# Kernel optimization log

Measured on AMD Instinct MI355X. Metric: run time of the kernel, lower is better.

The kernel has to match this reference:

```python
import jax, jax.numpy as jnp
import numpy as np

D = 1024; H = 16; DKV = 64; DFF = 4096
NB = 32; MAXD = 128
B = 4; LD = 1024; LE = 1024
NEG = -1e9
EPS = 1e-6


def setup_inputs():
    key = jax.random.key(0)
    ks = jax.random.split(key, 13)
    s = 0.02
    def W(k, shape):
        return jax.random.normal(k, shape, jnp.float32) * s
    return {
        "encoder_hidden_states": jax.random.normal(ks[0], (B, LE, D), jnp.float32),
        "hidden_states": jax.random.normal(ks[1], (B, LD, D), jnp.float32),
        "ln1_w": jnp.ones((D,), jnp.float32),
        "sa_q": W(ks[2], (D, H * DKV)),
        "sa_k": W(ks[3], (D, H * DKV)),
        "sa_v": W(ks[4], (D, H * DKV)),
        "sa_o": W(ks[5], (H * DKV, D)),
        "rel_bias": W(ks[6], (NB, H)),
        "ln2_w": jnp.ones((D,), jnp.float32),
        "ca_q": W(ks[7], (D, H * DKV)),
        "ca_k": W(ks[8], (D, H * DKV)),
        "ca_v": W(ks[9], (D, H * DKV)),
        "ca_o": W(ks[10], (H * DKV, D)),
        "ln3_w": jnp.ones((D,), jnp.float32),
        "wi": W(ks[11], (D, DFF)),
        "wo": W(ks[12], (DFF, D)),
        "final_ln_w": jnp.ones((D,), jnp.float32),
        "encoder_attention_mask": jnp.ones((B, LE), jnp.int32),
        "attention_mask": jnp.ones((B, LD), jnp.int32),
    }


def _rms(x, w):
    # T5 LayerNorm: RMS norm, no mean subtraction, no bias
    var = jnp.mean(x * x, axis=-1, keepdims=True)
    return x * jax.lax.rsqrt(var + EPS) * w


def _rel_bucket(rp):
    # T5 relative position bucketing, non-bidirectional (decoder causal)
    n = -jnp.minimum(rp, 0)
    max_exact = NB // 2
    is_small = n < max_exact
    nf = jnp.maximum(n, 1).astype(jnp.float32)
    val_large = max_exact + (
        jnp.log(nf / max_exact) / np.log(MAXD / max_exact) * (NB - max_exact)
    ).astype(jnp.int32)
    val_large = jnp.minimum(val_large, NB - 1)
    return jnp.where(is_small, n, val_large)


def _attn(xq, xkv, Wq, Wk, Wv, Wo, bias):
    b, lq, _ = xq.shape
    lk = xkv.shape[1]
    q = (xq @ Wq).reshape(b, lq, H, DKV)
    k = (xkv @ Wk).reshape(b, lk, H, DKV)
    v = (xkv @ Wv).reshape(b, lk, H, DKV)
    # T5: no 1/sqrt(d) scaling; additive position bias + mask before softmax
    scores = jnp.einsum('bqhd,bkhd->bhqk', q, k) + bias
    p = jax.nn.softmax(scores, axis=-1)
    o = jnp.einsum('bhqk,bkhd->bqhd', p, v).reshape(b, lq, H * DKV)
    return o @ Wo


def reference(encoder_hidden_states, hidden_states, ln1_w, sa_q, sa_k, sa_v, sa_o,
              rel_bias, ln2_w, ca_q, ca_k, ca_v, ca_o, ln3_w, wi, wo, final_ln_w,
              encoder_attention_mask, attention_mask):
    b, ld, _ = hidden_states.shape
    q_pos = jnp.arange(ld)[:, None]
    k_pos = jnp.arange(ld)[None, :]
    pos_bias = rel_bias[_rel_bucket(k_pos - q_pos)].transpose(2, 0, 1)[None]  # [1,H,LD,LD]
    # decoder extended mask: causal AND padding
    self_ok = (k_pos <= q_pos)[None, None] & (attention_mask[:, None, None, :] > 0)
    self_bias = pos_bias + jnp.where(self_ok, 0.0, NEG)
    # cross-attention: encoder padding mask; enc-dec position bias is zeros
    cross_bias = jnp.where(encoder_attention_mask[:, None, None, :] > 0, 0.0, NEG)

    h = hidden_states
    x = _rms(h, ln1_w)
    h = h + _attn(x, x, sa_q, sa_k, sa_v, sa_o, self_bias)
    x = _rms(h, ln2_w)
    h = h + _attn(x, encoder_hidden_states, ca_q, ca_k, ca_v, ca_o, cross_bias)
    x = _rms(h, ln3_w)
    h = h + jax.nn.relu(x @ wi) @ wo
    return _rms(h, final_ln_w)
```

## Files before the change

### kernel.cpp

```cpp
#include <hip/hip_runtime.h>


#define BB   4
#define LDEC 1024
#define LENC 1024
#define DIM  1024
#define NH   16
#define DK   64
#define DFFN 4096
#define NEGF (-1e9f)

typedef unsigned short u16;
typedef __attribute__((ext_vector_type(8))) unsigned short u16x8;
typedef __attribute__((ext_vector_type(8))) short s16x8;
typedef __attribute__((ext_vector_type(4))) float f32x4;

__device__ __forceinline__ float bf2f(u16 u) {
    union { unsigned int i; float f; } c; c.i = ((unsigned int)u) << 16; return c.f;
}
__device__ __forceinline__ u16 f2bf(float f) {
    union { float f; unsigned int i; } c; c.f = f;
    unsigned int x = c.i;
    return (u16)((x + 0x7fffu + ((x >> 16) & 1u)) >> 16);
}
__device__ __forceinline__ bool probe_f32(const void* probe) {
    return ((const u16*)probe)[0] != 0x3F80;
}
__device__ __forceinline__ float ldx(const void* p, long i, bool f32) {
    return f32 ? ((const float*)p)[i] : bf2f(((const u16*)p)[i]);
}
__device__ __forceinline__ float4 ldx4(const void* p, long i, bool f32) {
    if (f32) return ((const float4*)p)[i >> 2];
    ushort4 u = ((const ushort4*)p)[i >> 2];
    return make_float4(bf2f(u.x), bf2f(u.y), bf2f(u.z), bf2f(u.w));
}
__device__ __forceinline__ void stx(void* p, long i, float v, bool f32) {
    if (f32) ((float*)p)[i] = v;
    else     ((u16*)p)[i] = f2bf(v);
}

__device__ __forceinline__ void gload16(const void* g, void* l) {
    __builtin_amdgcn_global_load_lds(
        (const __attribute__((address_space(1))) void*)g,
        (__attribute__((address_space(3))) void*)l, 16, 0, 0);
}

__global__ __launch_bounds__(256) void copy_k(const void* __restrict__ src,
                                              void* __restrict__ dst,
                                              const void* __restrict__ probe, int n) {
    bool pf = probe_f32(probe);
    long bytes = (long)n * (pf ? 4 : 2);
    long off = ((long)blockIdx.x * 256 + threadIdx.x) * 16;
    if (off < bytes)
        *(int4*)((char*)dst + off) = *(const int4*)((const char*)src + off);
}

__global__ __launch_bounds__(256) void cvt_k(const void* __restrict__ src,
                                             u16* __restrict__ dst,
                                             const void* __restrict__ probe, int n4) {
    bool pf = probe_f32(probe);
    int i = blockIdx.x * 256 + threadIdx.x;
    if (i >= n4) return;
    if (pf) {
        float4 f = ((const float4*)src)[i];
        ushort4 o;
        o.x = f2bf(f.x); o.y = f2bf(f.y); o.z = f2bf(f.z); o.w = f2bf(f.w);
        ((ushort4*)dst)[i] = o;
    } else {
        ((ushort4*)dst)[i] = ((const ushort4*)src)[i];
    }
}

struct TPack {
    const void* s[10]; void* d[10];
    int K[10], N[10], t0[11];
};
__global__ __launch_bounds__(256) void transp_k(TPack p, const void* __restrict__ probe) {
    bool pf = probe_f32(probe);
    __shared__ u16 tl[32][33];
    int bid = blockIdx.x;
    int w = 0;
    while (bid >= p.t0[w + 1]) ++w;
    int lt = bid - p.t0[w];
    const int K = p.K[w], N = p.N[w];
    const int ntx = N >> 5;
    const int bn = (lt % ntx) * 32, bk = (lt / ntx) * 32;
    const int c = threadIdx.x & 31, rr = threadIdx.x >> 5;
    const void* s = p.s[w];
    u16* d = (u16*)p.d[w];
#pragma unroll
    for (int i = 0; i < 4; ++i) {
        int r = rr + i * 8;
        long gi = (long)(bk + r) * N + bn + c;
        tl[c][r] = pf ? f2bf(((const float*)s)[gi]) : ((const u16*)s)[gi];
    }
    __syncthreads();
#pragma unroll
    for (int i = 0; i < 4; ++i) {
        int r = rr + i * 8;
        d[(long)(bn + r) * K + bk + c] = tl[r][c];
    }
}

template <int XM, int YM, int CP>
__global__ __launch_bounds__(256) void rms_k(const void* __restrict__ X,
                                             const void* __restrict__ w,
                                             void* __restrict__ Y,
                                             void* __restrict__ R,
                                             const void* __restrict__ probe,
                                             long xoff, long yoff) {
    bool pf = probe_f32(probe);
    bool xf = XM && pf, yf = YM && pf;
    const int row = blockIdx.x, t = threadIdx.x;
    const long idx = (long)row * DIM + t * 4;
    float4 xv = ldx4(X, xoff + idx, xf);
    float ss = xv.x * xv.x;
    ss = fmaf(xv.y, xv.y, ss);
    ss = fmaf(xv.z, xv.z, ss);
    ss = fmaf(xv.w, xv.w, ss);
#pragma unroll
    for (int off = 32; off; off >>= 1) ss += __shfl_xor(ss, off, 64);
    __shared__ float part[4];
    if ((t & 63) == 0) part[t >> 6] = ss;
    __syncthreads();
    float tot = part[0] + part[1] + part[2] + part[3];
    float scale = rsqrtf(tot * (1.f / (float)DIM) + 1e-6f);
    float4 wv = ldx4(w, t * 4, pf);
    if (CP) {
        stx(R, idx + 0, xv.x, pf);
        stx(R, idx + 1, xv.y, pf);
        stx(R, idx + 2, xv.z, pf);
        stx(R, idx + 3, xv.w, pf);
    }
    stx(Y, yoff + idx + 0, xv.x * scale * wv.x, yf);
    stx(Y, yoff + idx + 1, xv.y * scale * wv.y, yf);
    stx(Y, yoff + idx + 2, xv.z * scale * wv.z, yf);
    stx(Y, yoff + idx + 3, xv.w * scale * wv.w, yf);
}

struct Gemm2Arg {
    const u16* A; const u16* BT; void* C;
    long aoff; long boff; long coff; int ldb;
};

template <int EPI, int BM>
__global__ __launch_bounds__(512) void mgemm2_k(Gemm2Arg g0, Gemm2Arg g1, Gemm2Arg g2,
                                                const void* __restrict__ probe,
                                                int M, int N, int K) {
    const bool pf = probe_f32(probe);
    Gemm2Arg ga = (blockIdx.z == 0) ? g0 : (blockIdx.z == 1 ? g1 : g2);
    constexpr int AG = BM / 64;
    constexpr int AFR = BM / 32;

    __shared__ u16 Asm[2][BM * 64];
    __shared__ u16 Bsm[2][128 * 64];

    const int tid = threadIdx.x;
    const int nx = gridDim.x;
    const int nwg = nx * gridDim.y;
    const int L = blockIdx.x + nx * blockIdx.y;
    const int tile = (L & 7) * (nwg >> 3) + (L >> 3);
    const int m_base = (tile / nx) * BM, n_base = (tile % nx) * 128;

    const int w = tid >> 6, lane = tid & 63;
    const int wm = w >> 2, wn = w & 3;
    const int l15 = lane & 15, quad = lane >> 4;
    const int arow8 = lane >> 3;
    const int acg = (lane & 7) ^ arow8;

    const int iters = K >> 6;
    const u16* Ab = ga.A + ga.aoff;
    const u16* Bb = ga.BT + ga.boff;

#pragma unroll
    for (int g = 0; g < AG; ++g)
        gload16(Ab + (long)(m_base + w * (BM / 8) + g * 8 + arow8) * K + acg * 8,
                &Asm[0][(w * (BM / 8) + g * 8) * 64]);
#pragma unroll
    for (int g = 0; g < 2; ++g)
        gload16(Bb + (long)(n_base + w * 16 + g * 8 + arow8) * ga.ldb + acg * 8,
                &Bsm[0][(w * 16 + g * 8) * 64]);

    f32x4 acc[AFR][2] = {};
    int cur = 0;
    for (int it = 0; it < iters; ++it) {
        __syncthreads();
        if (it + 1 < iters) {
            const int k0 = (it + 1) << 6;
#pragma unroll
            for (int g = 0; g < AG; ++g)
                gload16(Ab + (long)(m_base + w * (BM / 8) + g * 8 + arow8) * K + k0 + acg * 8,
                        &Asm[cur ^ 1][(w * (BM / 8) + g * 8) * 64]);
#pragma unroll
            for (int g = 0; g < 2; ++g)
                gload16(Bb + (long)(n_base + w * 16 + g * 8 + arow8) * ga.ldb + k0 + acg * 8,
                        &Bsm[cur ^ 1][(w * 16 + g * 8) * 64]);
        }
#pragma unroll
        for (int s = 0; s < 2; ++s) {
            s16x8 afr[AFR], bfr[2];
#pragma unroll
            for (int i = 0; i < AFR; ++i) {
                int row = wm * (BM / 2) + i * 16 + l15;
                int chunk = ((s << 2) | quad) ^ (row & 7);
                afr[i] = *(const s16x8*)&Asm[cur][row * 64 + chunk * 8];
            }
#pragma unroll
            for (int j = 0; j < 2; ++j) {
                int nr = wn * 32 + j * 16 + l15;
                int chunk = ((s << 2) | quad) ^ (nr & 7);
                bfr[j] = *(const s16x8*)&Bsm[cur][nr * 64 + chunk * 8];
            }
#pragma unroll
            for (int i = 0; i < AFR; ++i)
#pragma unroll
                for (int j = 0; j < 2; ++j)
                    acc[i][j] = __builtin_amdgcn_mfma_f32_16x16x32_bf16(
                        afr[i], bfr[j], acc[i][j], 0, 0, 0);
        }
        cur ^= 1;
    }

#pragma unroll
    for (int i = 0; i < AFR; ++i) {
#pragma unroll
        for (int j = 0; j < 2; ++j) {
            int n = n_base + wn * 32 + j * 16 + l15;
#pragma unroll
            for (int r4 = 0; r4 < 4; ++r4) {
                int m = m_base + wm * (BM / 2) + i * 16 + quad * 4 + r4;
                float v = acc[i][j][r4];
                if (EPI == 1) v = fmaxf(v, 0.f);
                long cidx = ga.coff + (long)m * N + n;
                if (EPI == 2) {
                    v += ldx(ga.C, cidx, pf);
                    stx(ga.C, cidx, v, pf);
                } else {
                    ((u16*)ga.C)[cidx] = f2bf(v);
                }
            }
        }
    }
}

struct GemmArg {
    const void* A; const void* B; void* C;
    long aoff; long boff; long coff; int asrc; int bsrc; int ldb;
};

__device__ __forceinline__ void load_breg(const GemmArg& ga, bool bf, int k0,
                                          int bk2, int bnb, int n_base, u16* breg) {
    long base0 = (long)(k0 + bk2) * ga.ldb + ga.boff + n_base + bnb;
    long base1 = base0 + ga.ldb;
    if (bf) {
        const float4* Bf = (const float4*)ga.B;
#pragma unroll
        for (int r = 0; r < 2; ++r) {
            long b = (r ? base1 : base0) >> 2;
#pragma unroll
            for (int c = 0; c < 2; ++c) {
                float4 f = Bf[b + c];
                breg[r * 8 + c * 4 + 0] = f2bf(f.x);
                breg[r * 8 + c * 4 + 1] = f2bf(f.y);
                breg[r * 8 + c * 4 + 2] = f2bf(f.z);
                breg[r * 8 + c * 4 + 3] = f2bf(f.w);
            }
        }
    } else {
        u16x8 v0 = *(const u16x8*)((const u16*)ga.B + base0);
        u16x8 v1 = *(const u16x8*)((const u16*)ga.B + base1);
#pragma unroll
        for (int i = 0; i < 8; ++i) { breg[i] = v0[i]; breg[8 + i] = v1[i]; }
    }
}

template <int EPI>
__global__ __launch_bounds__(512) void mgemm_k(GemmArg g0, GemmArg g1, GemmArg g2,
                                               const void* __restrict__ probe,
                                               int M, int N, int K) {
    const bool pf = probe_f32(probe);
    GemmArg ga = (blockIdx.z == 0) ? g0 : (blockIdx.z == 1 ? g1 : g2);
    const bool af = (ga.asrc >= 1) && pf;
    const bool bf = (ga.bsrc >= 1) && pf;

    __shared__ u16 Asm[2][128 * 64];
    __shared__ u16 Bsm[128 * 64];

    const int tid = threadIdx.x;
    const int nx = gridDim.x;
    const int nwg = nx * gridDim.y;
    const int L = blockIdx.x + nx * blockIdx.y;
    const int tile = (L & 7) * (nwg >> 3) + (L >> 3);
    const int m_base = (tile / nx) * 128, n_base = (tile % nx) * 128;

    const int w = tid >> 6, lane = tid & 63;
    const int wm = w >> 2, wn = w & 3;
    const int l15 = lane & 15, quad = lane >> 4;

    const int bk2 = (tid & 31) * 2;
    const int bnb = (tid >> 5) * 8;
    const int arow8 = lane >> 3;
    const int acg = (lane & 7) ^ arow8;

    const int iters = K >> 6;
    u16 breg[16];
    load_breg(ga, bf, 0, bk2, bnb, n_base, breg);
    if (!af) {
#pragma unroll
        for (int g = 0; g < 2; ++g) {
            const u16* Ag = (const u16*)ga.A + ga.aoff +
                            (long)(m_base + w * 16 + g * 8 + arow8) * K + acg * 8;
            gload16(Ag, &Asm[0][(w * 16 + g * 8) * 64]);
        }
    }

    f32x4 acc[4][2] = {};

    for (int it = 0; it < iters; ++it) {
        const int cur = it & 1;
        __syncthreads();
        if (af) {
            const int row = tid >> 2;
            const float4* Af = (const float4*)ga.A;
            long gb = ga.aoff + (long)(m_base + row) * K + (it << 6);
#pragma unroll
            for (int c = 0; c < 2; ++c) {
                int cg = (tid & 3) * 2 + c;
                float4 fa = Af[(gb + cg * 8) >> 2];
                float4 fb = Af[((gb + cg * 8) >> 2) + 1];
                u16x8 o;
                o[0] = f2bf(fa.x); o[1] = f2bf(fa.y); o[2] = f2bf(fa.z); o[3] = f2bf(fa.w);
                o[4] = f2bf(fb.x); o[5] = f2bf(fb.y); o[6] = f2bf(fb.z); o[7] = f2bf(fb.w);
                *(u16x8*)&Asm[cur][row * 64 + ((cg ^ (row & 7)) << 3)] = o;
            }
        }
#pragma unroll
        for (int i = 0; i < 8; ++i) {
            int n = bnb + i;
            unsigned int pr = (unsigned int)breg[i] | ((unsigned int)breg[8 + i] << 16);
            *(unsigned int*)&Bsm[n * 64 + (((bk2 >> 3) ^ (n & 7)) << 3) + (bk2 & 7)] = pr;
        }
        __syncthreads();
        if (it + 1 < iters) {
            load_breg(ga, bf, (it + 1) << 6, bk2, bnb, n_base, breg);
            if (!af) {
#pragma unroll
                for (int g = 0; g < 2; ++g) {
                    const u16* Ag = (const u16*)ga.A + ga.aoff +
                                    (long)(m_base + w * 16 + g * 8 + arow8) * K +
                                    ((it + 1) << 6) + acg * 8;
                    gload16(Ag, &Asm[cur ^ 1][(w * 16 + g * 8) * 64]);
                }
            }
        }
#pragma unroll
        for (int s = 0; s < 2; ++s) {
            s16x8 afr[4], bfr[2];
#pragma unroll
            for (int i = 0; i < 4; ++i) {
                int row = wm * 64 + i * 16 + l15;
                int chunk = ((s << 2) | quad) ^ (row & 7);
                afr[i] = *(const s16x8*)&Asm[cur][row * 64 + chunk * 8];
            }
#pragma unroll
            for (int j = 0; j < 2; ++j) {
                int nr = wn * 32 + j * 16 + l15;
                int chunk = ((s << 2) | quad) ^ (nr & 7);
                bfr[j] = *(const s16x8*)&Bsm[nr * 64 + chunk * 8];
            }
#pragma unroll
            for (int i = 0; i < 4; ++i)
#pragma unroll
                for (int j = 0; j < 2; ++j)
                    acc[i][j] = __builtin_amdgcn_mfma_f32_16x16x32_bf16(
                        afr[i], bfr[j], acc[i][j], 0, 0, 0);
        }
    }

#pragma unroll
    for (int i = 0; i < 4; ++i) {
#pragma unroll
        for (int j = 0; j < 2; ++j) {
            int n = n_base + wn * 32 + j * 16 + l15;
#pragma unroll
            for (int r4 = 0; r4 < 4; ++r4) {
                int m = m_base + wm * 64 + i * 16 + quad * 4 + r4;
                float v = acc[i][j][r4];
                if (EPI == 1) v = fmaxf(v, 0.f);
                long cidx = ga.coff + (long)m * N + n;
                if (EPI == 2) {
                    v += ldx(ga.C, cidx, pf);
                    stx(ga.C, cidx, v, pf);
                } else {
                    ((u16*)ga.C)[cidx] = f2bf(v);
                }
            }
        }
    }
}

template <int SELF>
__global__ __launch_bounds__(256) void fattn_k(const u16* __restrict__ Q,
                                               const u16* __restrict__ K,
                                               const u16* __restrict__ V,
                                               const void* __restrict__ relb,
                                               const int* __restrict__ mask,
                                               u16* __restrict__ O,
                                               const void* __restrict__ probe,
                                               int LK, int b0, int bufrows) {
    const bool pf = probe_f32(probe);
    __shared__ u16 Ks[64][72];
    __shared__ u16 Vt[64][72];
    __shared__ u16 Ps[64][72];
    __shared__ float bias_lut[SELF ? 1024 : 1];

    const int t = threadIdx.x;
    const int lane = t & 63, w = t >> 6;
    const int l15 = lane & 15, quad = lane >> 4;

    int x, h, z;
    if (gridDim.z == 4) {
        int lid = blockIdx.x + (int)gridDim.x * (blockIdx.y + (int)gridDim.y * blockIdx.z);
        int q = lid >> 8, r = lid & 255, a = r & 3;
        x = (q == 0) ? a : (q == 1) ? 15 - a : (q == 2) ? 4 + a : 11 - a;
        h = (r >> 2) & 15;
        z = r >> 6;
    } else {
        x = blockIdx.x; h = blockIdx.y; z = blockIdx.z;
    }
    const int q0 = x * 64;
    const int batch = b0 + z;
    const long bv = (long)z * bufrows * DIM;
    const int* mrow = mask + batch * LK;

    if (SELF) {
        for (int i = t; i < 1024; i += 256) {
            int bucket;
            if (i < 16) bucket = i;
            else {
                int vv = 16 + (int)(logf((float)i * 0.0625f) * 7.69436394f);
                bucket = vv < 31 ? vv : 31;
            }
            bias_lut[i] = ldx(relb, bucket * NH + h, pf);
        }
    }

    s16x8 qf[2];
    {
        const u16* qp = Q + bv + (long)(q0 + w * 16 + l15) * DIM + h * DK + quad * 8;
        qf[0] = *(const s16x8*)qp;
        qf[1] = *(const s16x8*)(qp + 32);
    }

    float l_reg[4] = {0.f, 0.f, 0.f, 0.f};
    f32x4 Oa[4] = {};

    const int ntiles = SELF ? (q0 >> 6) + 1 : (LK >> 6);
    const int kr = t >> 2, kseg = t & 3;
    const int kr2 = (t & 31) * 2, dnb = (t >> 5) * 8;

    u16x8 kp0, kp1, vp0, vp1;
    {
        long gb = bv + (long)kr * DIM + h * DK + kseg * 16;
        kp0 = *(const u16x8*)(K + gb);
        kp1 = *(const u16x8*)(K + gb + 8);
        long gv = bv + (long)kr2 * DIM + h * DK + dnb;
        vp0 = *(const u16x8*)(V + gv);
        vp1 = *(const u16x8*)(V + gv + DIM);
    }

    for (int kt = 0; kt < ntiles; ++kt) {
        __syncthreads();
        *(u16x8*)&Ks[kr][kseg * 16] = kp0;
        *(u16x8*)&Ks[kr][kseg * 16 + 8] = kp1;
#pragma unroll
        for (int i = 0; i < 8; ++i) {
            unsigned int pr = (unsigned int)vp0[i] | ((unsigned int)vp1[i] << 16);
            *(unsigned int*)&Vt[dnb + i][kr2] = pr;
        }
        __syncthreads();
        if (kt + 1 < ntiles) {
            long gb = bv + (long)((kt + 1) * 64 + kr) * DIM + h * DK + kseg * 16;
            kp0 = *(const u16x8*)(K + gb);
            kp1 = *(const u16x8*)(K + gb + 8);
            long gv = bv + (long)((kt + 1) * 64 + kr2) * DIM + h * DK + dnb;
            vp0 = *(const u16x8*)(V + gv);
            vp1 = *(const u16x8*)(V + gv + DIM);
        }

        f32x4 sc[4] = {};
#pragma unroll
        for (int j = 0; j < 4; ++j)
#pragma unroll
            for (int s = 0; s < 2; ++s) {
                s16x8 bf = *(const s16x8*)&Ks[j * 16 + l15][s * 32 + quad * 8];
                sc[j] = __builtin_amdgcn_mfma_f32_16x16x32_bf16(qf[s], bf, sc[j], 0, 0, 0);
            }

#pragma unroll
        for (int j = 0; j < 4; ++j) {
            int key = kt * 64 + j * 16 + l15;
            float ma = (mrow[key] > 0) ? 0.f : NEGF;
#pragma unroll
            for (int r = 0; r < 4; ++r) {
                float sv = sc[j][r];
                if (SELF) {
                    int q = q0 + w * 16 + quad * 4 + r;
                    int d = q - key;
                    sv += bias_lut[d < 0 ? 0 : d] + ((key <= q) ? ma : NEGF);
                } else {
                    sv += ma;
                }
                float p = __expf(sv);
                Ps[w * 16 + quad * 4 + r][j * 16 + l15] = f2bf(p);
                l_reg[r] += p;
            }
        }
        asm volatile("" ::: "memory");

#pragma unroll
        for (int s = 0; s < 2; ++s) {
            s16x8 pa = *(const s16x8*)&Ps[w * 16 + l15][s * 32 + quad * 8];
#pragma unroll
            for (int j = 0; j < 4; ++j) {
                s16x8 vb = *(const s16x8*)&Vt[j * 16 + l15][s * 32 + quad * 8];
                Oa[j] = __builtin_amdgcn_mfma_f32_16x16x32_bf16(pa, vb, Oa[j], 0, 0, 0);
            }
        }
    }

#pragma unroll
    for (int r = 0; r < 4; ++r) {
        float v = l_reg[r];
        v += __shfl_xor(v, 1, 64);
        v += __shfl_xor(v, 2, 64);
        v += __shfl_xor(v, 4, 64);
        v += __shfl_xor(v, 8, 64);
        l_reg[r] = 1.f / v;
    }
#pragma unroll
    for (int j = 0; j < 4; ++j)
#pragma unroll
        for (int r = 0; r < 4; ++r) {
            int row = w * 16 + quad * 4 + r;
            O[bv + (long)(q0 + row) * DIM + h * DK + j * 16 + l15] =
                f2bf(Oa[j][r] * l_reg[r]);
        }
}

extern "C" void kernel_launch(void* const* d_in, const int* in_sizes, int n_in,
                              void* d_out, int out_size, void* d_ws, size_t ws_size,
                              hipStream_t stream) {
    const void* enc  = d_in[0];
    const void* hs   = d_in[1];
    const void* ln1  = d_in[2];
    const void* sa_q = d_in[3];
    const void* sa_k = d_in[4];
    const void* sa_v = d_in[5];
    const void* sa_o = d_in[6];
    const void* relb = d_in[7];
    const void* ln2  = d_in[8];
    const void* ca_q = d_in[9];
    const void* ca_k = d_in[10];
    const void* ca_v = d_in[11];
    const void* ca_o = d_in[12];
    const void* ln3  = d_in[13];
    const void* wi   = d_in[14];
    const void* wo   = d_in[15];
    const void* fln  = d_in[16];
    const int* enc_mask = (const int*)d_in[17];
    const int* dec_mask = (const int*)d_in[18];
    void* out = d_out;
    const void* probe = ln1;

    char* ws = (char*)d_ws;
    const int M = BB * LDEC;
    dim3 blk(256), blkG(512);
    GemmArg dz = {nullptr, nullptr, nullptr, 0, 0, 0, 0, 0, 0};
    Gemm2Arg dz2 = {nullptr, nullptr, nullptr, 0, 0, 0, 0};

    if (ws_size >= (72ull << 20)) {
        u16* X0 = (u16*)(ws);
        u16* X1 = (u16*)(ws + (8u  << 20));
        u16* X2 = (u16*)(ws + (16u << 20));
        u16* X3 = (u16*)(ws + (24u << 20));
        u16* FF = X1;
        u16* encB = (u16*)(ws + (32u << 20));
        u16* wT[10];
        wT[0] = (u16*)(ws + (40u << 20));
        wT[1] = (u16*)(ws + (42u << 20));
        wT[2] = (u16*)(ws + (44u << 20));
        wT[3] = (u16*)(ws + (46u << 20));
        wT[4] = (u16*)(ws + (48u << 20));
        wT[5] = (u16*)(ws + (50u << 20));
        wT[6] = (u16*)(ws + (52u << 20));
        wT[7] = (u16*)(ws + (54u << 20));
        wT[8] = (u16*)(ws + (56u << 20));
        wT[9] = (u16*)(ws + (64u << 20));

        cvt_k<<<4096, blk, 0, stream>>>(enc, encB, probe, 1048576);
        {
            TPack p;
            const void* s[10] = {sa_q, sa_k, sa_v, sa_o, ca_q, ca_k, ca_v, ca_o, wi, wo};
            const int kk[10] = {DIM, DIM, DIM, DIM, DIM, DIM, DIM, DIM, DIM, DFFN};
            const int nn[10] = {DIM, DIM, DIM, DIM, DIM, DIM, DIM, DIM, DFFN, DIM};
            int acc = 0;
            for (int i = 0; i < 10; ++i) {
                p.s[i] = s[i]; p.d[i] = wT[i]; p.K[i] = kk[i]; p.N[i] = nn[i];
                p.t0[i] = acc; acc += (kk[i] >> 5) * (nn[i] >> 5);
            }
            p.t0[10] = acc;
            transp_k<<<acc, blk, 0, stream>>>(p, probe);
        }

        dim3 gQKV(8, 64, 3);
        dim3 gOP(8, 64, 1);
        dim3 gWI(16, 64, 2);
        dim3 gAttn(LDEC / 64, NH, BB);

        rms_k<1, 0, 1><<<M, blk, 0, stream>>>(hs, ln1, X0, out, probe, 0, 0);
        {
            Gemm2Arg zq = {X0, wT[0], X1, 0, 0, 0, DIM};
            Gemm2Arg zk = {X0, wT[1], X2, 0, 0, 0, DIM};
            Gemm2Arg zv = {X0, wT[2], X3, 0, 0, 0, DIM};
            mgemm2_k<0, 64><<<gQKV, blkG, 0, stream>>>(zq, zk, zv, probe, M, DIM, DIM);
        }
        fattn_k<1><<<gAttn, blk, 0, stream>>>(X1, X2, X3, relb, dec_mask, X0,
                                              probe, LDEC, 0, LDEC);
        {
            Gemm2Arg zo = {X0, wT[3], out, 0, 0, 0, DIM};
            mgemm2_k<2, 64><<<gOP, blkG, 0, stream>>>(zo, dz2, dz2, probe, M, DIM, DIM);
        }

        rms_k<1, 0, 0><<<M, blk, 0, stream>>>(out, ln2, X0, nullptr, probe, 0, 0);
        {
            Gemm2Arg zq = {X0, wT[4], X1, 0, 0, 0, DIM};
            Gemm2Arg zk = {encB, wT[5], X2, 0, 0, 0, DIM};
            Gemm2Arg zv = {encB, wT[6], X3, 0, 0, 0, DIM};
            mgemm2_k<0, 64><<<gQKV, blkG, 0, stream>>>(zq, zk, zv, probe, M, DIM, DIM);
        }
        fattn_k<0><<<gAttn, blk, 0, stream>>>(X1, X2, X3, relb, enc_mask, X0,
                                              probe, LENC, 0, LENC);
        {
            Gemm2Arg zo = {X0, wT[7], out, 0, 0, 0, DIM};
            mgemm2_k<2, 64><<<gOP, blkG, 0, stream>>>(zo, dz2, dz2, probe, M, DIM, DIM);
        }

        rms_k<1, 0, 0><<<M, blk, 0, stream>>>(out, ln3, X0, nullptr, probe, 0, 0);
        {
            Gemm2Arg z0 = {X0, wT[8], FF, 0, 0, 0, DIM};
            Gemm2Arg z1 = {X0, wT[8], FF, 0, (long)2048 * DIM, 2048, DIM};
            mgemm2_k<1, 64><<<gWI, blkG, 0, stream>>>(z0, z1, dz2, probe, M, DFFN, DIM);
        }
        {
            Gemm2Arg zo = {FF, wT[9], out, 0, 0, 0, DFFN};
            mgemm2_k<2, 64><<<gOP, blkG, 0, stream>>>(zo, dz2, dz2, probe, M, DIM, DFFN);
        }
    } else if (ws_size >= (32ull << 20)) {
        u16* X0 = (u16*)(ws);
        u16* X1 = (u16*)(ws + (8u << 20));
        u16* X2 = (u16*)(ws + (16u << 20));
        u16* X3 = (u16*)(ws + (24u << 20));
        u16* FF = X2;
        const bool have_encb = ws_size >= (40ull << 20);
        u16* encB = (u16*)(ws + (32u << 20));

        dim3 gQKV(8, 32, 3);
        dim3 gOP(8, 32, 1);
        dim3 gWI(16, 32, 1);
        dim3 gAttn(LDEC / 64, NH, BB);

        copy_k<<<(M * DIM / 4) / 256, blk, 0, stream>>>(hs, out, probe, M * DIM);
        if (have_encb)
            cvt_k<<<4096, blk, 0, stream>>>(enc, encB, probe, M * DIM / 4);

        rms_k<1, 0, 0><<<M, blk, 0, stream>>>(out, ln1, X0, nullptr, probe, 0, 0);
        {
            GemmArg zq = {X0, sa_q, X1, 0, 0, 0, 0, 1, DIM};
            GemmArg zk = {X0, sa_k, X2, 0, 0, 0, 0, 1, DIM};
            GemmArg zv = {X0, sa_v, X3, 0, 0, 0, 0, 1, DIM};
            mgemm_k<0><<<gQKV, blkG, 0, stream>>>(zq, zk, zv, probe, M, DIM, DIM);
        }
        fattn_k<1><<<gAttn, blk, 0, stream>>>(X1, X2, X3, relb, dec_mask, X0,
                                              probe, LDEC, 0, LDEC);
        {
            GemmArg zo = {X0, sa_o, out, 0, 0, 0, 0, 1, DIM};
            mgemm_k<2><<<gOP, blkG, 0, stream>>>(zo, dz, dz, probe, M, DIM, DIM);
        }

        rms_k<1, 0, 0><<<M, blk, 0, stream>>>(out, ln2, X0, nullptr, probe, 0, 0);
        {
            const void* encA = have_encb ? (const void*)encB : enc;
            int asrc = have_encb ? 0 : 1;
            GemmArg zq = {X0, ca_q, X1, 0, 0, 0, 0, 1, DIM};
            GemmArg zk = {encA, ca_k, X2, 0, 0, 0, asrc, 1, DIM};
            GemmArg zv = {encA, ca_v, X3, 0, 0, 0, asrc, 1, DIM};
            mgemm_k<0><<<gQKV, blkG, 0, stream>>>(zq, zk, zv, probe, M, DIM, DIM);
        }
        fattn_k<0><<<gAttn, blk, 0, stream>>>(X1, X2, X3, relb, enc_mask, X0,
                                              probe, LENC, 0, LENC);
        {
            GemmArg zo = {X0, ca_o, out, 0, 0, 0, 0, 1, DIM};
            mgemm_k<2><<<gOP, blkG, 0, stream>>>(zo, dz, dz, probe, M, DIM, DIM);
        }

        rms_k<1, 0, 0><<<M, blk, 0, stream>>>(out, ln3, X0, nullptr, probe, 0, 0);
        for (int d = 0; d < 2; ++d) {
            GemmArg zi = {X0, wi, FF, 0, (long)d * 2048, 0, 0, 1, DFFN};
            mgemm_k<1><<<gWI, blkG, 0, stream>>>(zi, dz, dz, probe, M, 2048, DIM);
            GemmArg zo = {FF, wo, out, 0, (long)d * 2048 * DIM, 0, 0, 1, DIM};
            mgemm_k<2><<<gOP, blkG, 0, stream>>>(zo, dz, dz, probe, M, DIM, 2048);
        }
    } else {
        u16* X0 = (u16*)(ws);
        u16* X1 = (u16*)(ws + (2u << 20));
        u16* X2 = (u16*)(ws + (4u << 20));
        u16* X3 = (u16*)(ws + (6u << 20));
        u16* XN = (u16*)(ws);
        u16* FF = (u16*)(ws + (4u << 20));
        dim3 gQKV(8, 8, 3);
        dim3 gOP(8, 8, 1);
        dim3 gFFN(8, 16, 1);
        dim3 gAttn(LDEC / 64, NH, 1);

        copy_k<<<(M * DIM / 4) / 256, blk, 0, stream>>>(hs, out, probe, M * DIM);

        for (int b = 0; b < BB; ++b) {
            const long ob = (long)b * LDEC * DIM;
            const long eb = (long)b * LENC * DIM;

            rms_k<1, 0, 0><<<LDEC, blk, 0, stream>>>(out, ln1, X0, nullptr, probe, ob, 0);
            {
                GemmArg zq = {X0, sa_q, X1, 0, 0, 0, 0, 1, DIM};
                GemmArg zk = {X0, sa_k, X2, 0, 0, 0, 0, 1, DIM};
                GemmArg zv = {X0, sa_v, X3, 0, 0, 0, 0, 1, DIM};
                mgemm_k<0><<<gQKV, blkG, 0, stream>>>(zq, zk, zv, probe, LDEC, DIM, DIM);
            }
            fattn_k<1><<<gAttn, blk, 0, stream>>>(X1, X2, X3, relb, dec_mask, X0,
                                                  probe, LDEC, b, 0);
            {
                GemmArg zo = {X0, sa_o, out, 0, 0, ob, 0, 1, DIM};
                mgemm_k<2><<<gOP, blkG, 0, stream>>>(zo, dz, dz, probe, LDEC, DIM, DIM);
            }

            rms_k<1, 0, 0><<<LDEC, blk, 0, stream>>>(out, ln2, X0, nullptr, probe, ob, 0);
            {
                GemmArg zq = {X0, ca_q, X1, 0, 0, 0, 0, 1, DIM};
                GemmArg zk = {enc, ca_k, X2, eb, 0, 0, 1, 1, DIM};
                GemmArg zv = {enc, ca_v, X3, eb, 0, 0, 1, 1, DIM};
                mgemm_k<0><<<gQKV, blkG, 0, stream>>>(zq, zk, zv, probe, LENC, DIM, DIM);
            }
            fattn_k<0><<<gAttn, blk, 0, stream>>>(X1, X2, X3, relb, enc_mask, X0,
                                                  probe, LENC, b, 0);
            {
                GemmArg zo = {X0, ca_o, out, 0, 0, ob, 0, 1, DIM};
                mgemm_k<2><<<gOP, blkG, 0, stream>>>(zo, dz, dz, probe, LDEC, DIM, DIM);
            }
        }

        for (int mc = 0; mc < 2; ++mc) {
            const long r0 = (long)mc * 2048;
            rms_k<1, 0, 0><<<2048, blk, 0, stream>>>(out, ln3, XN, nullptr, probe, r0 * DIM, 0);
            for (int d = 0; d < 4; ++d) {
                GemmArg zi = {XN, wi, FF, 0, (long)d * 1024, 0, 0, 1, DFFN};
                mgemm_k<1><<<gFFN, blkG, 0, stream>>>(zi, dz, dz, probe, 2048, 1024, DIM);
                GemmArg zo = {FF, wo, out, 0, (long)d * 1024 * DIM, r0 * DIM, 0, 1, DIM};
                mgemm_k<2><<<gFFN, blkG, 0, stream>>>(zo, dz, dz, probe, 2048, DIM, 1024);
            }
        }
    }

    rms_k<1, 1, 0><<<M, blk, 0, stream>>>(out, fln, out, nullptr, probe, 0, 0);
}
```

Baseline: 508.7 us.

## Triple-buffer GEMM shared memory with explicit vmcnt waits and raw barrier

```diff
diff --git a/kernel.cpp b/kernel.cpp
--- a/kernel.cpp
+++ b/kernel.cpp
@@ -151,9 +151,10 @@
     Gemm2Arg ga = (blockIdx.z == 0) ? g0 : (blockIdx.z == 1 ? g1 : g2);
     constexpr int AG = BM / 64;
     constexpr int AFR = BM / 32;
-
-    __shared__ u16 Asm[2][BM * 64];
-    __shared__ u16 Bsm[2][128 * 64];
+    static_assert(BM == 64, "vmcnt literal assumes 3 loads/tile");
+
+    __shared__ u16 Asm[3][BM * 64];
+    __shared__ u16 Bsm[3][128 * 64];
 
     const int tid = threadIdx.x;
     const int nx = gridDim.x;
@@ -172,30 +173,33 @@
     const u16* Ab = ga.A + ga.aoff;
     const u16* Bb = ga.BT + ga.boff;
 
-#pragma unroll
-    for (int g = 0; g < AG; ++g)
-        gload16(Ab + (long)(m_base + w * (BM / 8) + g * 8 + arow8) * K + acg * 8,
-                &Asm[0][(w * (BM / 8) + g * 8) * 64]);
-#pragma unroll
-    for (int g = 0; g < 2; ++g)
-        gload16(Bb + (long)(n_base + w * 16 + g * 8 + arow8) * ga.ldb + acg * 8,
-                &Bsm[0][(w * 16 + g * 8) * 64]);
+    auto issue = [&](int it, int buf) {
+        const int k0 = it << 6;
+#pragma unroll
+        for (int g = 0; g < AG; ++g)
+            gload16(Ab + (long)(m_base + w * (BM / 8) + g * 8 + arow8) * K + k0 + acg * 8,
+                    &Asm[buf][(w * (BM / 8) + g * 8) * 64]);
+#pragma unroll
+        for (int g = 0; g < 2; ++g)
+            gload16(Bb + (long)(n_base + w * 16 + g * 8 + arow8) * ga.ldb + k0 + acg * 8,
+                    &Bsm[buf][(w * 16 + g * 8) * 64]);
+    };
+
+    issue(0, 0);
+    if (iters > 1) issue(1, 1);
 
     f32x4 acc[AFR][2] = {};
     int cur = 0;
     for (int it = 0; it < iters; ++it) {
-        __syncthreads();
-        if (it + 1 < iters) {
-            const int k0 = (it + 1) << 6;
-#pragma unroll
-            for (int g = 0; g < AG; ++g)
-                gload16(Ab + (long)(m_base + w * (BM / 8) + g * 8 + arow8) * K + k0 + acg * 8,
-                        &Asm[cur ^ 1][(w * (BM / 8) + g * 8) * 64]);
-#pragma unroll
-            for (int g = 0; g < 2; ++g)
-                gload16(Bb + (long)(n_base + w * 16 + g * 8 + arow8) * ga.ldb + k0 + acg * 8,
-                        &Bsm[cur ^ 1][(w * 16 + g * 8) * 64]);
-        }
+        if (it + 1 < iters) asm volatile("s_waitcnt vmcnt(3)" ::: "memory");
+        else                asm volatile("s_waitcnt vmcnt(0)" ::: "memory");
+        asm volatile("s_barrier" ::: "memory");
+        if (it + 2 < iters) {
+            int nb = cur + 2; if (nb >= 3) nb -= 3;
+            issue(it + 2, nb);
+        }
+        const u16* As = Asm[cur];
+        const u16* Bs = Bsm[cur];
 #pragma unroll
         for (int s = 0; s < 2; ++s) {
             s16x8 afr[AFR], bfr[2];
@@ -203,13 +207,13 @@
             for (int i = 0; i < AFR; ++i) {
                 int row = wm * (BM / 2) + i * 16 + l15;
                 int chunk = ((s << 2) | quad) ^ (row & 7);
-                afr[i] = *(const s16x8*)&Asm[cur][row * 64 + chunk * 8];
+                afr[i] = *(const s16x8*)&As[row * 64 + chunk * 8];
             }
 #pragma unroll
             for (int j = 0; j < 2; ++j) {
                 int nr = wn * 32 + j * 16 + l15;
                 int chunk = ((s << 2) | quad) ^ (nr & 7);
-                bfr[j] = *(const s16x8*)&Bsm[cur][nr * 64 + chunk * 8];
+                bfr[j] = *(const s16x8*)&Bs[nr * 64 + chunk * 8];
             }
 #pragma unroll
             for (int i = 0; i < AFR; ++i)
@@ -218,7 +222,7 @@
                     acc[i][j] = __builtin_amdgcn_mfma_f32_16x16x32_bf16(
                         afr[i], bfr[j], acc[i][j], 0, 0, 0);
         }
-        cur ^= 1;
+        if (++cur == 3) cur = 0;
     }
 
 #pragma unroll
```

Measured after the change: 535.0 us. +5.2%, slower.
